# Kernel tuning notes

Measured on AMD Instinct MI355X. Metric: run time of the kernel, lower is better.

## Reference

```python
import jax, jax.numpy as jnp
import numpy as np

KS = 7                 # sconv_kernel_size
PAD = (KS - 1) // 2
SIMS_SCALE = 10.0      # sims_norm_scale
EPS = 1e-5


def setup_inputs() -> dict:
    key = jax.random.key(0)
    k1, k2, k3, k4 = jax.random.split(key, 4)
    T, C, H, W = 4, 3, 192, 192
    S = 300
    x = jax.random.normal(k1, (T, C, H, W), jnp.float32)
    spix = jax.random.randint(k2, (T, H, W), 0, S, dtype=jnp.int32)
    W_lin = jax.random.normal(k3, (C, C * KS * KS), jnp.float32) * 0.05
    b_lin = jax.random.normal(k4, (C,), jnp.float32) * 0.05
    return {"x": x, "spix": spix, "W_lin": W_lin, "b_lin": b_lin, "n_spix": S}


def _get_sims(x, spix, n_spix, scale):
    # x: [T,C,H,W], spix: [T,H,W] with contiguous ids in [0, n_spix)
    T, C, H, W = x.shape
    feats = x.transpose(0, 2, 3, 1).reshape(T, H * W, C)   # t (h w) f
    ids = spix.reshape(T, H * W)

    def pool(f, i):
        s = jax.ops.segment_sum(f, i, num_segments=n_spix)                      # [S,C]
        c = jax.ops.segment_sum(jnp.ones((f.shape[0],), f.dtype), i, num_segments=n_spix)  # [S]
        return s / jnp.maximum(c, 1.0)[:, None], c

    means, cnt = jax.vmap(pool)(feats, ids)                # [T,S,C], [T,S]
    # squared euclidean distance (cdist ** 2)
    d2 = (jnp.sum(feats * feats, -1)[:, :, None]
          + jnp.sum(means * means, -1)[:, None, :]
          - 2.0 * jnp.einsum('tnc,tsc->tns', feats, means))
    d2 = jnp.maximum(d2, 0.0)                              # [T,HW,S]
    # superpixels absent from frame t get distance inf (pwd[mask] = inf)
    d2 = jnp.where((cnt > 0)[:, None, :], d2, jnp.inf)
    sims = jax.nn.softmax(-scale * d2, axis=-1)            # softmax over superpixels
    return sims.reshape(T, H, W, n_spix)                   # [T,H,W,S]


def _prod_attn(sims):
    # non-local 'prod' search, zero flow, ws=KS: dot product of sims vectors
    # between each pixel and its KSxKS neighborhood (zero-padded borders)
    T, H, W, S = sims.shape
    p = jnp.pad(sims, ((0, 0), (PAD, PAD), (PAD, PAD), (0, 0)))
    attn = [jnp.einsum('thws,thws->thw', sims, p[:, dy:dy + H, dx:dx + W, :])
            for dy in range(KS) for dx in range(KS)]
    return jnp.stack(attn, -1)                             # [T,H,W,KS*KS]


def _unfold(x):
    # torch.nn.Unfold(kernel_size=KS, padding=PAD): zero pad, row-major window
    T, C, H, W = x.shape
    p = jnp.pad(x, ((0, 0), (0, 0), (PAD, PAD), (PAD, PAD)))
    pats = [p[:, :, dy:dy + H, dx:dx + W] for dy in range(KS) for dx in range(KS)]
    return jnp.stack(pats, 2)                              # [T,C,KS*KS,H,W]


def reference(x, spix, W_lin, b_lin, n_spix):
    T, C, H, W = x.shape
    sims = _get_sims(x, spix, n_spix, SIMS_SCALE)          # [T,H,W,S]
    rw = _prod_attn(sims)                                  # [T,H,W,K2]
    # apply_norm('max'): divide by max over neighborhood
    rw = rw / (EPS + jnp.max(rw, axis=-1, keepdims=True))
    Wk = W_lin.reshape(W_lin.shape[0], C, KS * KS)         # [od,id,k2]
    pats = _unfold(x)                                      # [T,id,k2,H,W]
    # out[t,o,h,w] = sum_{i,k} W[o,i,k] * rw[t,h,w,k] * patch[t,i,k,h,w] + b[o]
    out = jnp.einsum('oik,thwk,tikhw->tohw', Wk, rw, pats) + b_lin[None, :, None, None]
    return out
```

## Files before the change

### kernel.cpp

```cpp
#include <hip/hip_runtime.h>
#include <math.h>

#define TT 4
#define HH 192
#define WW 192
#define SS 300
#define SP 320
#define HW (HH*WW)
#define PD 3
#define TSW 12
#define TSH 16
#define HLW 18
#define HLH 22
#define NHP (HLH*HLW)
#define PSTRG 400
#define NSEG 48
#define MEANS 360448
#define MOFF 393216

typedef _Float16 h8 __attribute__((ext_vector_type(8)));
typedef float f4 __attribute__((ext_vector_type(4)));


__launch_bounds__(256)
__global__ void k_accum(const float* __restrict__ x, const int* __restrict__ spix,
                        float* __restrict__ ws) {
    __shared__ float ls[SS * 4];
    const int tid = threadIdx.x;
    const int t = blockIdx.y, seg = blockIdx.x;
    for (int i = tid; i < SS * 4; i += 256) ls[i] = 0.f;
    __syncthreads();
#pragma unroll
    for (int it = 0; it < 3; it++) {
        int px = seg * 768 + it * 256 + tid;
        int s = spix[t * HW + px];
        atomicAdd(&ls[s * 4 + 0], x[(t * 3 + 0) * HW + px]);
        atomicAdd(&ls[s * 4 + 1], x[(t * 3 + 1) * HW + px]);
        atomicAdd(&ls[s * 4 + 2], x[(t * 3 + 2) * HW + px]);
        atomicAdd(&ls[s * 4 + 3], 1.f);
    }
    __syncthreads();
    float* part = ws + (t * NSEG + seg) * 1200;
    for (int i = tid; i < SS * 4; i += 256) part[i] = ls[i];
}

__launch_bounds__(256)
__global__ void k_prep(const float* __restrict__ x, float* __restrict__ ws) {
    __shared__ float4 sm[SP];
    const int tid = threadIdx.x;
    const int t = blockIdx.y;
    const float* part = ws + t * NSEG * 1200;
    for (int i = tid; i < SP; i += 256) {
        float4 m;
        if (i < SS) {
            float s0 = 0.f, s1 = 0.f, s2 = 0.f, c = 0.f;
            for (int g = 0; g < NSEG; g++) {
                s0 += part[g * 1200 + i * 4 + 0];
                s1 += part[g * 1200 + i * 4 + 1];
                s2 += part[g * 1200 + i * 4 + 2];
                c  += part[g * 1200 + i * 4 + 3];
            }
            float inv = 1.f / fmaxf(c, 1.f);
            float mx = s0 * inv, my = s1 * inv, mz = s2 * inv;
            m.x = 20.f * mx; m.y = 20.f * my; m.z = 20.f * mz;
            m.w = (c > 0.f) ? (-10.f * (mx * mx + my * my + mz * mz)) : -INFINITY;
        } else {
            m.x = 0.f; m.y = 0.f; m.z = 0.f; m.w = -INFINITY;
        }
        sm[i] = m;
        if (blockIdx.x == 0) ((float4*)(ws + MEANS))[t * SP + i] = m;
    }
    __syncthreads();

    const int p0 = blockIdx.x * 768 + tid;
    const int p1 = p0 + 256, p2 = p0 + 512;
    const float f0x = x[(t * 3 + 0) * HW + p0], f0y = x[(t * 3 + 1) * HW + p0], f0z = x[(t * 3 + 2) * HW + p0];
    const float f1x = x[(t * 3 + 0) * HW + p1], f1y = x[(t * 3 + 1) * HW + p1], f1z = x[(t * 3 + 2) * HW + p1];
    const float f2x = x[(t * 3 + 0) * HW + p2], f2y = x[(t * 3 + 1) * HW + p2], f2z = x[(t * 3 + 2) * HW + p2];

    float M0 = -INFINITY, M1 = -INFINITY, M2 = -INFINITY;
#pragma unroll 4
    for (int s = 0; s < SS; s++) {
        float4 a = sm[s];
        M0 = fmaxf(M0, fmaf(f0x, a.x, fmaf(f0y, a.y, fmaf(f0z, a.z, a.w))));
        M1 = fmaxf(M1, fmaf(f1x, a.x, fmaf(f1y, a.y, fmaf(f1z, a.z, a.w))));
        M2 = fmaxf(M2, fmaf(f2x, a.x, fmaf(f2y, a.y, fmaf(f2z, a.z, a.w))));
    }
    float Z0 = 0.f, Z1 = 0.f, Z2 = 0.f;
#pragma unroll 4
    for (int s = 0; s < SS; s++) {
        float4 a = sm[s];
        Z0 += __expf(fmaf(f0x, a.x, fmaf(f0y, a.y, fmaf(f0z, a.z, a.w))) - M0);
        Z1 += __expf(fmaf(f1x, a.x, fmaf(f1y, a.y, fmaf(f1z, a.z, a.w))) - M1);
        Z2 += __expf(fmaf(f2x, a.x, fmaf(f2y, a.y, fmaf(f2z, a.z, a.w))) - M2);
    }
    float2* mzt = (float2*)(ws + MOFF) + t * HW;
    mzt[p0] = make_float2(M0, 1.f / Z0);
    mzt[p1] = make_float2(M1, 1.f / Z1);
    mzt[p2] = make_float2(M2, 1.f / Z2);
}

#define REP49(M) M(0)M(1)M(2)M(3)M(4)M(5)M(6)M(7)M(8)M(9)M(10)M(11)M(12)M(13) \
    M(14)M(15)M(16)M(17)M(18)M(19)M(20)M(21)M(22)M(23)M(24)M(25)M(26)M(27) \
    M(28)M(29)M(30)M(31)M(32)M(33)M(34)M(35)M(36)M(37)M(38)M(39)M(40)M(41) \
    M(42)M(43)M(44)M(45)M(46)M(47)M(48)

#define QOFF(k) (((k) / 7 - PD) * HLW + ((k) % 7 - PD))


__launch_bounds__(512, 2)
__global__ void k_main(const float* __restrict__ x, const float* __restrict__ Wlin,
                       const float* __restrict__ blin, const float* __restrict__ ws,
                       float* __restrict__ out) {
    __shared__ __align__(16) char ebuf[2][8 * PSTRG * 16];
    __shared__ float4 sfh[NHP];
    __shared__ float  sW[441];
    __shared__ float4 smean[SP];

    const int tid = threadIdx.x;
    const int wid = tid >> 6, lane = tid & 63;
    const int pxc = lane & 15, kg = lane >> 4;
    const int t = blockIdx.z;
    const int gx0 = blockIdx.x * TSW - PD, gy0 = blockIdx.y * TSH - PD;
    const float4* m4 = (const float4*)(ws + MEANS) + t * SP;

    for (int i = tid; i < 441; i += 512) sW[i] = Wlin[i];
    for (int i = tid; i < SP; i += 512) smean[i] = m4[i];

    float fx = 0.f, fy = 0.f, fz = 0.f, M = INFINITY;
    if (tid < NHP) {
        int hy = tid / HLW, hx = tid - hy * HLW;
        int gy = gy0 + hy, gx = gx0 + hx;
        float iZ = 0.f;
        if (gy >= 0 && gy < HH && gx >= 0 && gx < WW) {
            int p = gy * WW + gx;
            fx = x[(t * 3 + 0) * HW + p];
            fy = x[(t * 3 + 1) * HW + p];
            fz = x[(t * 3 + 2) * HW + p];
            float2 mz = ((const float2*)(ws + MOFF))[t * HW + p];
            M  = mz.x;
            iZ = mz.y;
        }
        sfh[tid] = make_float4(fx, fy, fz, iZ);
    }
    __syncthreads();

#define PHASEB(cc, bb) if (tid < NHP) { \
        char* dst = ebuf[bb]; \
        _Pragma("unroll") \
        for (int jd = 0; jd < 8; jd++) { \
            h8 v; \
            _Pragma("unroll") \
            for (int e = 0; e < 4; e++) { \
                float4 ma = smean[(cc) * 64 + jd * 8 + 2 * e]; \
                float4 mb = smean[(cc) * 64 + jd * 8 + 2 * e + 1]; \
                float E0 = __expf(fmaf(fx, ma.x, fmaf(fy, ma.y, fmaf(fz, ma.z, ma.w))) - M); \
                float E1 = __expf(fmaf(fx, mb.x, fmaf(fy, mb.y, fmaf(fz, mb.z, mb.w))) - M); \
                auto pr = __builtin_amdgcn_cvt_pkrtz(E0, E1); \
                v[2 * e] = (_Float16)pr.x; v[2 * e + 1] = (_Float16)pr.y; \
            } \
            *(h8*)(dst + (jd * PSTRG + tid) * 16) = v; \
        } }

    const int r0 = 2 * wid;
    const int acol = (pxc > 14) ? 14 : pxc;
    const int gA0 = kg * PSTRG + (r0 + PD) * HLW + PD + acol;
    const int gA1 = gA0 + HLW;
    const int bcol2 = (16 + pxc > 17) ? 17 : 16 + pxc;
    const int gB1 = kg * PSTRG + r0 * HLW + pxc;
    const int gB2 = kg * PSTRG + r0 * HLW + bcol2;

    f4 zero4 = {0.f, 0.f, 0.f, 0.f};
    f4 aP[7], aQ[7], aR[7], aS[7];
#pragma unroll
    for (int d = 0; d < 7; d++) { aP[d] = zero4; aQ[d] = zero4; aR[d] = zero4; aS[d] = zero4; }

#define MFMA_STEP(pbk) { \
        h8 A0 = *(const h8*)((pbk) + gA0 * 16); \
        h8 A1 = *(const h8*)((pbk) + gA1 * 16); \
        h8 c1 = *(const h8*)((pbk) + gB1 * 16); \
        h8 c2 = *(const h8*)((pbk) + gB2 * 16); \
        h8 n1 = *(const h8*)((pbk) + (gB1 + HLW) * 16); \
        h8 n2 = *(const h8*)((pbk) + (gB2 + HLW) * 16); \
        aP[0] = __builtin_amdgcn_mfma_f32_16x16x32_f16(A0, c1, aP[0], 0, 0, 0); \
        aQ[0] = __builtin_amdgcn_mfma_f32_16x16x32_f16(A0, c2, aQ[0], 0, 0, 0); \
        _Pragma("unroll") \
        for (int d = 1; d < 7; d++) { \
            h8 f1 = *(const h8*)((pbk) + (gB1 + (d + 1) * HLW) * 16); \
            h8 f2 = *(const h8*)((pbk) + (gB2 + (d + 1) * HLW) * 16); \
            aP[d]     = __builtin_amdgcn_mfma_f32_16x16x32_f16(A0, n1, aP[d], 0, 0, 0); \
            aR[d - 1] = __builtin_amdgcn_mfma_f32_16x16x32_f16(A1, n1, aR[d - 1], 0, 0, 0); \
            aQ[d]     = __builtin_amdgcn_mfma_f32_16x16x32_f16(A0, n2, aQ[d], 0, 0, 0); \
            aS[d - 1] = __builtin_amdgcn_mfma_f32_16x16x32_f16(A1, n2, aS[d - 1], 0, 0, 0); \
            n1 = f1; n2 = f2; \
        } \
        aR[6] = __builtin_amdgcn_mfma_f32_16x16x32_f16(A1, n1, aR[6], 0, 0, 0); \
        aS[6] = __builtin_amdgcn_mfma_f32_16x16x32_f16(A1, n2, aS[6], 0, 0, 0); }

#define MFMA_CHUNK { \
        __builtin_amdgcn_s_setprio(1); \
        MFMA_STEP(pb) \
        MFMA_STEP(pb + 4 * PSTRG * 16) \
        __builtin_amdgcn_s_setprio(0); }

    PHASEB(0, 0)

#pragma unroll 1
    for (int c = 0; c < 5; c++) {
        __syncthreads();
        const char* pb = ebuf[c & 1];
        if (wid & 1) {
            MFMA_CHUNK
            if (c < 4) { PHASEB(c + 1, (c + 1) & 1) }
        } else {
            if (c < 4) { PHASEB(c + 1, (c + 1) & 1) }
            MFMA_CHUNK
        }
    }
    __syncthreads();

    float* attn = (float*)ebuf;
#pragma unroll
    for (int d = 0; d < 7; d++) {
#pragma unroll
        for (int reg = 0; reg < 4; reg++) {
            int i = 4 * kg + reg;
            int u1 = pxc - i;
            int u2 = u1 + 16;
            if (i < TSW) {
                if ((unsigned)u1 <= 6u) {
                    attn[(r0 * TSW + i) * 51 + d * 7 + u1] = aP[d][reg];
                    attn[((r0 + 1) * TSW + i) * 51 + d * 7 + u1] = aR[d][reg];
                }
                if ((unsigned)u2 <= 6u) {
                    attn[(r0 * TSW + i) * 51 + d * 7 + u2] = aQ[d][reg];
                    attn[((r0 + 1) * TSW + i) * 51 + d * 7 + u2] = aS[d][reg];
                }
            }
        }
    }
    __syncthreads();

    if (tid < TSH * TSW) {
        const int r = tid / TSW, cq = tid - r * TSW;
        const int own = (r + PD) * HLW + (cq + PD);
        const float* ap = attn + tid * 51;
        float mx = 0.f;
#define PK1(k) mx = fmaxf(mx, ap[k] * sfh[own + QOFF(k)].w);
        REP49(PK1)
#undef PK1
        const float iZp = sfh[own].w;
        const float inv = 1.f / (1e-5f / iZp + mx);

        float o0 = blin[0], o1 = blin[1], o2 = blin[2];
#define PK2(k) { float4 f = sfh[own + QOFF(k)]; \
        float rwk = ap[k] * f.w * inv; \
        o0 += rwk * (sW[k] * f.x + sW[49 + (k)] * f.y + sW[98 + (k)] * f.z); \
        o1 += rwk * (sW[147 + (k)] * f.x + sW[196 + (k)] * f.y + sW[245 + (k)] * f.z); \
        o2 += rwk * (sW[294 + (k)] * f.x + sW[343 + (k)] * f.y + sW[392 + (k)] * f.z); }
        REP49(PK2)
#undef PK2

        int p = (gy0 + PD + r) * WW + gx0 + PD + cq;
        out[(t * 3 + 0) * HW + p] = o0;
        out[(t * 3 + 1) * HW + p] = o1;
        out[(t * 3 + 2) * HW + p] = o2;
    }
}

extern "C" void kernel_launch(void* const* d_in, const int* in_sizes, int n_in,
                              void* d_out, int out_size, void* d_ws, size_t ws_size,
                              hipStream_t stream) {
    (void)in_sizes; (void)n_in; (void)out_size; (void)ws_size;
    const float* x    = (const float*)d_in[0];
    const int*   spix = (const int*)d_in[1];
    const float* Wlin = (const float*)d_in[2];
    const float* blin = (const float*)d_in[3];
    float* out = (float*)d_out;
    float* ws  = (float*)d_ws;

    hipLaunchKernelGGL(k_accum, dim3(NSEG, TT), dim3(256), 0, stream, x, spix, ws);
    hipLaunchKernelGGL(k_prep,  dim3(HW / 768, TT), dim3(256), 0, stream, x, ws);
    hipLaunchKernelGGL(k_main,  dim3(WW / TSW, HH / TSH, TT), dim3(512), 0, stream,
                       x, Wlin, blin, ws, out);
}
```

Before: 112.1 us.

## Halve k_main tile height, split exp work across two thread halves, raise occupancy

Shrinks the main kernel's output tile from 16 to 8 rows, so each wave computes one row with half as many MFMA accumulators. The smaller halo and exp buffer let the launch bounds ask for 4 blocks per CU instead of 2. The softmax-exp staging is now spread over two thread halves, each covering half the superpixel slice, and the loop runs 10 chunks of 32 superpixels instead of 5 of 64. In exchange the halo overhead per output pixel is higher (14x18 halo for 8x12 outputs), more barriers are needed, and the grid launch must change to match.

```diff
diff --git a/kernel.cpp b/kernel.cpp
--- a/kernel.cpp
+++ b/kernel.cpp
@@ -9,11 +9,11 @@
 #define HW (HH*WW)
 #define PD 3
 #define TSW 12
-#define TSH 16
+#define TSH 8
 #define HLW 18
-#define HLH 22
+#define HLH 14
 #define NHP (HLH*HLW)
-#define PSTRG 400
+#define PSTRG 254
 #define NSEG 48
 #define MEANS 360448
 #define MOFF 393216
@@ -108,11 +108,11 @@
 #define QOFF(k) (((k) / 7 - PD) * HLW + ((k) % 7 - PD))
 
 
-__launch_bounds__(512, 2)
+__launch_bounds__(512, 4)
 __global__ void k_main(const float* __restrict__ x, const float* __restrict__ Wlin,
                        const float* __restrict__ blin, const float* __restrict__ ws,
                        float* __restrict__ out) {
-    __shared__ __align__(16) char ebuf[2][8 * PSTRG * 16];
+    __shared__ __align__(16) char ebuf[2][4 * PSTRG * 16];
     __shared__ float4 sfh[NHP];
     __shared__ float  sW[441];
     __shared__ float4 smean[SP];
@@ -127,93 +127,84 @@
     for (int i = tid; i < 441; i += 512) sW[i] = Wlin[i];
     for (int i = tid; i < SP; i += 512) smean[i] = m4[i];
 
+    const int half = (tid >= NHP) ? 1 : 0;
+    const int hp = tid - half * NHP;
     float fx = 0.f, fy = 0.f, fz = 0.f, M = INFINITY;
-    if (tid < NHP) {
-        int hy = tid / HLW, hx = tid - hy * HLW;
+    if (tid < 2 * NHP) {
+        int hy = hp / HLW, hx = hp - hy * HLW;
         int gy = gy0 + hy, gx = gx0 + hx;
-        float iZ = 0.f;
         if (gy >= 0 && gy < HH && gx >= 0 && gx < WW) {
             int p = gy * WW + gx;
             fx = x[(t * 3 + 0) * HW + p];
             fy = x[(t * 3 + 1) * HW + p];
             fz = x[(t * 3 + 2) * HW + p];
             float2 mz = ((const float2*)(ws + MOFF))[t * HW + p];
-            M  = mz.x;
-            iZ = mz.y;
-        }
-        sfh[tid] = make_float4(fx, fy, fz, iZ);
-    }
-    __syncthreads();
-
-#define PHASEB(cc, bb) if (tid < NHP) { \
+            M = mz.x;
+            if (half == 0) sfh[hp] = make_float4(fx, fy, fz, mz.y);
+        } else if (half == 0) {
+            sfh[hp] = make_float4(0.f, 0.f, 0.f, 0.f);
+        }
+    }
+    __syncthreads();
+
+#define PHASEB(cc, bb) if (tid < 2 * NHP) { \
         char* dst = ebuf[bb]; \
         _Pragma("unroll") \
-        for (int jd = 0; jd < 8; jd++) { \
+        for (int j2 = 0; j2 < 2; j2++) { \
+            int jd = 2 * half + j2; \
             h8 v; \
             _Pragma("unroll") \
             for (int e = 0; e < 4; e++) { \
-                float4 ma = smean[(cc) * 64 + jd * 8 + 2 * e]; \
-                float4 mb = smean[(cc) * 64 + jd * 8 + 2 * e + 1]; \
+                float4 ma = smean[(cc) * 32 + jd * 8 + 2 * e]; \
+                float4 mb = smean[(cc) * 32 + jd * 8 + 2 * e + 1]; \
                 float E0 = __expf(fmaf(fx, ma.x, fmaf(fy, ma.y, fmaf(fz, ma.z, ma.w))) - M); \
                 float E1 = __expf(fmaf(fx, mb.x, fmaf(fy, mb.y, fmaf(fz, mb.z, mb.w))) - M); \
                 auto pr = __builtin_amdgcn_cvt_pkrtz(E0, E1); \
                 v[2 * e] = (_Float16)pr.x; v[2 * e + 1] = (_Float16)pr.y; \
             } \
-            *(h8*)(dst + (jd * PSTRG + tid) * 16) = v; \
+            *(h8*)(dst + (jd * PSTRG + hp) * 16) = v; \
         } }
 
-    const int r0 = 2 * wid;
+    const int r = wid;
     const int acol = (pxc > 14) ? 14 : pxc;
-    const int gA0 = kg * PSTRG + (r0 + PD) * HLW + PD + acol;
-    const int gA1 = gA0 + HLW;
+    const int gA0 = kg * PSTRG + (r + PD) * HLW + PD + acol;
     const int bcol2 = (16 + pxc > 17) ? 17 : 16 + pxc;
-    const int gB1 = kg * PSTRG + r0 * HLW + pxc;
-    const int gB2 = kg * PSTRG + r0 * HLW + bcol2;
+    const int gB1 = kg * PSTRG + r * HLW + pxc;
+    const int gB2 = kg * PSTRG + r * HLW + bcol2;
 
     f4 zero4 = {0.f, 0.f, 0.f, 0.f};
-    f4 aP[7], aQ[7], aR[7], aS[7];
-#pragma unroll
-    for (int d = 0; d < 7; d++) { aP[d] = zero4; aQ[d] = zero4; aR[d] = zero4; aS[d] = zero4; }
-
-#define MFMA_STEP(pbk) { \
-        h8 A0 = *(const h8*)((pbk) + gA0 * 16); \
-        h8 A1 = *(const h8*)((pbk) + gA1 * 16); \
-        h8 c1 = *(const h8*)((pbk) + gB1 * 16); \
-        h8 c2 = *(const h8*)((pbk) + gB2 * 16); \
-        h8 n1 = *(const h8*)((pbk) + (gB1 + HLW) * 16); \
-        h8 n2 = *(const h8*)((pbk) + (gB2 + HLW) * 16); \
-        aP[0] = __builtin_amdgcn_mfma_f32_16x16x32_f16(A0, c1, aP[0], 0, 0, 0); \
-        aQ[0] = __builtin_amdgcn_mfma_f32_16x16x32_f16(A0, c2, aQ[0], 0, 0, 0); \
+    f4 aP[7], aQ[7];
+#pragma unroll
+    for (int d = 0; d < 7; d++) { aP[d] = zero4; aQ[d] = zero4; }
+
+#define MFMA_CHUNK { \
+        __builtin_amdgcn_s_setprio(1); \
+        h8 A0 = *(const h8*)(pb + gA0 * 16); \
+        h8 n1 = *(const h8*)(pb + gB1 * 16); \
+        h8 n2 = *(const h8*)(pb + gB2 * 16); \
         _Pragma("unroll") \
-        for (int d = 1; d < 7; d++) { \
-            h8 f1 = *(const h8*)((pbk) + (gB1 + (d + 1) * HLW) * 16); \
-            h8 f2 = *(const h8*)((pbk) + (gB2 + (d + 1) * HLW) * 16); \
-            aP[d]     = __builtin_amdgcn_mfma_f32_16x16x32_f16(A0, n1, aP[d], 0, 0, 0); \
-            aR[d - 1] = __builtin_amdgcn_mfma_f32_16x16x32_f16(A1, n1, aR[d - 1], 0, 0, 0); \
-            aQ[d]     = __builtin_amdgcn_mfma_f32_16x16x32_f16(A0, n2, aQ[d], 0, 0, 0); \
-            aS[d - 1] = __builtin_amdgcn_mfma_f32_16x16x32_f16(A1, n2, aS[d - 1], 0, 0, 0); \
+        for (int d = 0; d < 6; d++) { \
+            h8 f1 = *(const h8*)(pb + (gB1 + (d + 1) * HLW) * 16); \
+            h8 f2 = *(const h8*)(pb + (gB2 + (d + 1) * HLW) * 16); \
+            aP[d] = __builtin_amdgcn_mfma_f32_16x16x32_f16(A0, n1, aP[d], 0, 0, 0); \
+            aQ[d] = __builtin_amdgcn_mfma_f32_16x16x32_f16(A0, n2, aQ[d], 0, 0, 0); \
             n1 = f1; n2 = f2; \
         } \
-        aR[6] = __builtin_amdgcn_mfma_f32_16x16x32_f16(A1, n1, aR[6], 0, 0, 0); \
-        aS[6] = __builtin_amdgcn_mfma_f32_16x16x32_f16(A1, n2, aS[6], 0, 0, 0); }
-
-#define MFMA_CHUNK { \
-        __builtin_amdgcn_s_setprio(1); \
-        MFMA_STEP(pb) \
-        MFMA_STEP(pb + 4 * PSTRG * 16) \
+        aP[6] = __builtin_amdgcn_mfma_f32_16x16x32_f16(A0, n1, aP[6], 0, 0, 0); \
+        aQ[6] = __builtin_amdgcn_mfma_f32_16x16x32_f16(A0, n2, aQ[6], 0, 0, 0); \
         __builtin_amdgcn_s_setprio(0); }
 
     PHASEB(0, 0)
 
 #pragma unroll 1
-    for (int c = 0; c < 5; c++) {
+    for (int c = 0; c < 10; c++) {
         __syncthreads();
         const char* pb = ebuf[c & 1];
         if (wid & 1) {
             MFMA_CHUNK
-            if (c < 4) { PHASEB(c + 1, (c + 1) & 1) }
+            if (c < 9) { PHASEB(c + 1, (c + 1) & 1) }
         } else {
-            if (c < 4) { PHASEB(c + 1, (c + 1) & 1) }
+            if (c < 9) { PHASEB(c + 1, (c + 1) & 1) }
             MFMA_CHUNK
         }
     }
@@ -228,22 +219,16 @@
             int u1 = pxc - i;
             int u2 = u1 + 16;
             if (i < TSW) {
-                if ((unsigned)u1 <= 6u) {
-                    attn[(r0 * TSW + i) * 51 + d * 7 + u1] = aP[d][reg];
-                    attn[((r0 + 1) * TSW + i) * 51 + d * 7 + u1] = aR[d][reg];
-                }
-                if ((unsigned)u2 <= 6u) {
-                    attn[(r0 * TSW + i) * 51 + d * 7 + u2] = aQ[d][reg];
-                    attn[((r0 + 1) * TSW + i) * 51 + d * 7 + u2] = aS[d][reg];
-                }
+                if ((unsigned)u1 <= 6u) attn[(r * TSW + i) * 51 + d * 7 + u1] = aP[d][reg];
+                if ((unsigned)u2 <= 6u) attn[(r * TSW + i) * 51 + d * 7 + u2] = aQ[d][reg];
             }
         }
     }
     __syncthreads();
 
     if (tid < TSH * TSW) {
-        const int r = tid / TSW, cq = tid - r * TSW;
-        const int own = (r + PD) * HLW + (cq + PD);
+        const int rr = tid / TSW, cq = tid - rr * TSW;
+        const int own = (rr + PD) * HLW + (cq + PD);
         const float* ap = attn + tid * 51;
         float mx = 0.f;
 #define PK1(k) mx = fmaxf(mx, ap[k] * sfh[own + QOFF(k)].w);
@@ -261,7 +246,7 @@
         REP49(PK2)
 #undef PK2
 
-        int p = (gy0 + PD + r) * WW + gx0 + PD + cq;
+        int p = (gy0 + PD + rr) * WW + gx0 + PD + cq;
         out[(t * 3 + 0) * HW + p] = o0;
         out[(t * 3 + 1) * HW + p] = o1;
         out[(t * 3 + 2) * HW + p] = o2;
```

Result: slower. 165.6 us (+47.7%).
